# Kernel tuning notes

Hardware: AMD Instinct MI355X
Metric: run time of the kernel (lower is better)

## Reference

```python
import jax, jax.numpy as jnp
import numpy as np
from jax import lax

B, C, H, W = 16, 256, 32, 32
DH = 32
HEADS = C // DH          # 8
WSZ = 4                  # window size
K = 4                    # top-k windows
MR = 4                   # mlp_ratio
NWIN = (H // WSZ) * (W // WSZ)  # 64
WS = WSZ * WSZ                  # 16 tokens per window
EPS = 1e-5


def setup_inputs() -> dict:
    key = jax.random.key(0)
    ks = jax.random.split(key, 8)
    w = lambda i, shape: jax.random.normal(ks[i], shape, jnp.float32) * 0.02
    d = {
        'x': jax.random.normal(ks[0], (B, C, H, W), jnp.float32),
        'bn0_g': jax.random.uniform(ks[1], (C,), jnp.float32, 0.5, 1.5),
        'bn0_b': jnp.zeros((C,), jnp.float32),
        'bn0_m': jnp.zeros((C,), jnp.float32),
        'bn0_v': jnp.ones((C,), jnp.float32),
        'w_qkv': w(2, (3 * C, C)),
        'w_merge': w(3, (C, C)),
        'b_merge': jnp.zeros((C,), jnp.float32),
        'w1': w(4, (MR * C, C)),
        'bn1_g': jax.random.uniform(ks[5], (MR * C,), jnp.float32, 0.5, 1.5),
        'bn1_b': jnp.zeros((MR * C,), jnp.float32),
        'bn1_m': jnp.zeros((MR * C,), jnp.float32),
        'bn1_v': jnp.ones((MR * C,), jnp.float32),
        'dw': w(6, (MR * C, 1, 3, 3)),
        'bn2_g': jax.random.uniform(ks[7], (MR * C,), jnp.float32, 0.5, 1.5),
        'bn2_b': jnp.zeros((MR * C,), jnp.float32),
        'bn2_m': jnp.zeros((MR * C,), jnp.float32),
        'bn2_v': jnp.ones((MR * C,), jnp.float32),
        'w2': w(0, (C, MR * C)),
        'bn3_g': jax.random.uniform(ks[1], (C,), jnp.float32, 0.5, 1.5),
        'bn3_b': jnp.zeros((C,), jnp.float32),
        'bn3_m': jnp.zeros((C,), jnp.float32),
        'bn3_v': jnp.ones((C,), jnp.float32),
    }
    return d


def _bn(x, g, b, m, v):
    # eval-mode BatchNorm2d on NCHW
    s = (g / jnp.sqrt(v + EPS))
    return (x - m[None, :, None, None]) * s[None, :, None, None] + b[None, :, None, None]


def _win(t):
    # [B, C, H, W] -> [B, HEADS, NWIN, WS, DH]
    nh, nw = H // WSZ, W // WSZ
    t = t.reshape(B, HEADS, DH, nh, WSZ, nw, WSZ)
    return t.transpose(0, 1, 3, 5, 4, 6, 2).reshape(B, HEADS, NWIN, WS, DH)


def _unwin(t):
    # [B, HEADS, NWIN, WS, DH] -> [B, C, H, W]
    nh, nw = H // WSZ, W // WSZ
    t = t.reshape(B, HEADS, nh, nw, WSZ, WSZ, DH)
    return t.transpose(0, 1, 6, 2, 4, 3, 5).reshape(B, C, H, W)


def _forward(x, bn0_g, bn0_b, bn0_m, bn0_v, w_qkv, w_merge, b_merge,
             w1, bn1_g, bn1_b, bn1_m, bn1_v, dw, bn2_g, bn2_b, bn2_m, bn2_v,
             w2, bn3_g, bn3_b, bn3_m, bn3_v):
    # qkv projection: BN -> GELU -> 1x1 conv (no bias)
    h = jax.nn.gelu(_bn(x, bn0_g, bn0_b, bn0_m, bn0_v), approximate=False)
    qkv = jnp.einsum('oc,bchw->bohw', w_qkv, h)
    q, k, v = jnp.split(qkv, 3, axis=1)

    qw, kw, vw = _win(q), _win(k), _win(v)  # [B,H,NWIN,WS,DH]
    scale = 1.0 / jnp.sqrt(jnp.float32(DH))

    # window-level descriptors -> window-window affinity -> top-k selection
    wsc = jnp.einsum('bhid,bhjd->bhij', qw.mean(3), kw.mean(3)) * scale
    idx = lax.top_k(wsc, K)[1]  # [B,H,NWIN,K]

    # gather top-k kv windows per query window (irregular access)
    gather = jax.vmap(jax.vmap(lambda t, ix: t[ix]))  # over B, HEADS
    kk = gather(kw, idx).reshape(B, HEADS, NWIN, K * WS, DH)
    vv = gather(vw, idx).reshape(B, HEADS, NWIN, K * WS, DH)

    attn = jax.nn.softmax(jnp.einsum('bhnqd,bhnkd->bhnqk', qw, kk) * scale, axis=-1)
    msg = jnp.einsum('bhnqk,bhnkd->bhnqd', attn, vv)
    msg = _unwin(msg)

    # merge (1x1 conv with bias) + residual
    x = x + jnp.einsum('oc,bchw->bohw', w_merge, msg) + b_merge[None, :, None, None]

    # MB mlp: 1x1 expand -> BN -> GELU -> depthwise 3x3 -> BN -> GELU -> 1x1 -> BN
    h = jnp.einsum('oc,bchw->bohw', w1, x)
    h = jax.nn.gelu(_bn(h, bn1_g, bn1_b, bn1_m, bn1_v), approximate=False)
    h = lax.conv_general_dilated(h, dw, (1, 1), 'SAME',
                                 feature_group_count=MR * C,
                                 dimension_numbers=('NCHW', 'OIHW', 'NCHW'))
    h = jax.nn.gelu(_bn(h, bn2_g, bn2_b, bn2_m, bn2_v), approximate=False)
    h = jnp.einsum('oc,bchw->bohw', w2, h)
    h = _bn(h, bn3_g, bn3_b, bn3_m, bn3_v)
    return x + h


def reference(x, bn0_g, bn0_b, bn0_m, bn0_v, w_qkv, w_merge, b_merge,
              w1, bn1_g, bn1_b, bn1_m, bn1_v, dw, bn2_g, bn2_b, bn2_m, bn2_v,
              w2, bn3_g, bn3_b, bn3_m, bn3_v):
    return _forward(x, bn0_g, bn0_b, bn0_m, bn0_v, w_qkv, w_merge, b_merge,
                    w1, bn1_g, bn1_b, bn1_m, bn1_v, dw, bn2_g, bn2_b, bn2_m, bn2_v,
                    w2, bn3_g, bn3_b, bn3_m, bn3_v)
```

## Files before the change

### kernel.cpp

```cpp
#include <hip/hip_runtime.h>
#include <hip/hip_bf16.h>

#define EPSV 1e-5f

typedef short bf16x8 __attribute__((ext_vector_type(8)));
typedef float f32x4 __attribute__((ext_vector_type(4)));

__device__ __forceinline__ float gelu_f(float x) {
    return 0.5f * x * (1.0f + erff(x * 0.70710678118654752f));
}
__device__ __forceinline__ float b2f(unsigned short u) {
    union { float f; unsigned i; } c; c.i = ((unsigned)u) << 16; return c.f;
}
__device__ __forceinline__ unsigned short f2b(float f) {
    __hip_bfloat16 h = __float2bfloat16(f);
    return *reinterpret_cast<unsigned short*>(&h);
}
__device__ __forceinline__ float lo16f(unsigned v) {
    union { float f; unsigned i; } c; c.i = v << 16; return c.f;
}
__device__ __forceinline__ float hi16f(unsigned v) {
    union { float f; unsigned i; } c; c.i = v & 0xffff0000u; return c.f;
}
__device__ __forceinline__ void gload16(const unsigned short* g, unsigned short* l) {
    __builtin_amdgcn_global_load_lds(
        (const __attribute__((address_space(1))) void*)g,
        (__attribute__((address_space(3))) void*)l, 16, 0, 0);
}

__global__ __launch_bounds__(256) void wcvt_k(const float* __restrict__ w,
                                              unsigned short* __restrict__ o, int n4) {
    int i = blockIdx.x * 256 + threadIdx.x;
    if (i >= n4) return;
    float4 v = ((const float4*)w)[i];
    ushort4 u = make_ushort4(f2b(v.x), f2b(v.y), f2b(v.z), f2b(v.w));
    ((ushort4*)o)[i] = u;
}

__global__ __launch_bounds__(256) void wprep_k(const float* __restrict__ wdw,
    const float* __restrict__ g, const float* __restrict__ bt,
    const float* __restrict__ mu, const float* __restrict__ va,
    float* __restrict__ wt, float* __restrict__ scf, float* __restrict__ shf) {
    int ch = blockIdx.x * 256 + threadIdx.x;
    #pragma unroll
    for (int tap = 0; tap < 9; ++tap)
        wt[tap * 1024 + ch] = wdw[ch * 9 + tap];
    float s = g[ch] * rsqrtf(va[ch] + EPSV);
    scf[ch] = s;
    shf[ch] = bt[ch] - mu[ch] * s;
}

__global__ __launch_bounds__(256) void bn0tr_k(const float* __restrict__ x,
    const float* __restrict__ g, const float* __restrict__ bt,
    const float* __restrict__ mu, const float* __restrict__ va,
    unsigned short* __restrict__ h0b, float* __restrict__ xt) {
    __shared__ float tile[64][65];
    int hw0 = blockIdx.x * 64, c0 = blockIdx.y * 64, b = blockIdx.z;
    int t = threadIdx.x;
    int cl = t >> 6, hl = t & 63;
    #pragma unroll
    for (int r = 0; r < 16; ++r)
        tile[r * 4 + cl][hl] = x[((size_t)(b * 256 + c0 + r * 4 + cl)) * 1024 + hw0 + hl];
    __syncthreads();
    int c = c0 + (t & 63);
    float s = g[c] * rsqrtf(va[c] + EPSV);
    float m_ = mu[c], be = bt[c];
    #pragma unroll
    for (int r = 0; r < 16; ++r) {
        int hl2 = r * 4 + (t >> 6);
        float v = tile[t & 63][hl2];
        size_t o = ((size_t)(b * 1024 + hw0 + hl2)) * 256 + c;
        xt[o] = v;
        h0b[o] = f2b(gelu_f((v - m_) * s + be));
    }
}

__global__ __launch_bounds__(256) void hm_k(const float* __restrict__ xt,
    const float* __restrict__ g, const float* __restrict__ bt,
    const float* __restrict__ mu, const float* __restrict__ va,
    float* __restrict__ hm) {
    int blk = blockIdx.x;
    int b = blk >> 6, win = blk & 63;
    int c = threadIdx.x;
    int base = (win >> 3) * 128 + (win & 7) * 4;
    float s = g[c] * rsqrtf(va[c] + EPSV);
    float m_ = mu[c], be = bt[c];
    float acc = 0.f;
    #pragma unroll
    for (int ty = 0; ty < 4; ++ty)
        #pragma unroll
        for (int tx = 0; tx < 4; ++tx) {
            float v = xt[((size_t)(b * 1024 + base + ty * 32 + tx)) * 256 + c];
            acc += gelu_f((v - m_) * s + be);
        }
    hm[(size_t)blk * 256 + c] = acc * (1.f / 16.f);
}

template <int MODE>
__global__ __launch_bounds__(256) void mgemm(
    const unsigned short* __restrict__ A, const unsigned short* __restrict__ X,
    unsigned short* __restrict__ outb, float* __restrict__ outf,
    const float* __restrict__ res,
    const float* __restrict__ p0, const float* __restrict__ p1,
    const float* __restrict__ p2, const float* __restrict__ p3,
    int M, int Kd) {
    __shared__ __align__(16) unsigned short As[4096];
    __shared__ __align__(16) unsigned short Bs[4096];
    const int t = threadIdx.x;
    const int wid = t >> 6, lane = t & 63;
    const int n0 = blockIdx.x * 128, m0 = blockIdx.y * 128, b = blockIdx.z;
    const unsigned short* Ab = A + (size_t)m0 * Kd;
    const unsigned short* Xb = X + ((size_t)b * 1024 + n0) * Kd;

    const int srow = lane >> 2;
    const int skb  = (lane & 3) * 8;
    const int wr = wid >> 1, wc = wid & 1;
    const int lr = lane & 15;
    const int lk = (lane >> 4) * 8;

    f32x4 acc[4][4] = {};

    for (int k0 = 0; k0 < Kd; k0 += 32) {
        #pragma unroll
        for (int i = 0; i < 2; ++i) {
            int chunk = wid * 2 + i;
            int row = chunk * 16 + srow;
            gload16(Ab + (size_t)row * Kd + k0 + skb, &As[chunk * 512]);
            gload16(Xb + (size_t)row * Kd + k0 + skb, &Bs[chunk * 512]);
        }
        __syncthreads();
        bf16x8 af[4], bfv[4];
        #pragma unroll
        for (int mi = 0; mi < 4; ++mi)
            af[mi] = *(const bf16x8*)&As[(wr * 64 + mi * 16 + lr) * 32 + lk];
        #pragma unroll
        for (int ni = 0; ni < 4; ++ni)
            bfv[ni] = *(const bf16x8*)&Bs[(wc * 64 + ni * 16 + lr) * 32 + lk];
        #pragma unroll
        for (int mi = 0; mi < 4; ++mi)
            #pragma unroll
            for (int ni = 0; ni < 4; ++ni)
                acc[mi][ni] = __builtin_amdgcn_mfma_f32_16x16x32_bf16(
                    af[mi], bfv[ni], acc[mi][ni], 0, 0, 0);
        __syncthreads();
    }

    const int crow = (lane >> 4) * 4;
    #pragma unroll
    for (int ni = 0; ni < 4; ++ni) {
        const int n = n0 + wc * 64 + ni * 16 + lr;
        #pragma unroll
        for (int mi = 0; mi < 4; ++mi) {
            const int m = m0 + wr * 64 + mi * 16 + crow;
            f32x4 v = acc[mi][ni];
            size_t o = ((size_t)b * 1024 + n) * (size_t)M + m;
            if (MODE == 0) {
                *(ushort4*)(outb + o) = make_ushort4(f2b(v[0]), f2b(v[1]), f2b(v[2]), f2b(v[3]));
            } else if (MODE == 1) {
                float4 r = *(const float4*)(res + o);
                float4 bi = *(const float4*)(p0 + m);
                float w0 = v[0] + r.x + bi.x, w1 = v[1] + r.y + bi.y;
                float w2 = v[2] + r.z + bi.z, w3 = v[3] + r.w + bi.w;
                *(float4*)(outf + o) = make_float4(w0, w1, w2, w3);
                *(ushort4*)(outb + o) = make_ushort4(f2b(w0), f2b(w1), f2b(w2), f2b(w3));
            } else if (MODE == 2) {
                float4 gg = *(const float4*)(p0 + m);
                float4 be = *(const float4*)(p1 + m);
                float4 mm = *(const float4*)(p2 + m);
                float4 vv = *(const float4*)(p3 + m);
                float h0 = gelu_f((v[0] - mm.x) * (gg.x * rsqrtf(vv.x + EPSV)) + be.x);
                float h1 = gelu_f((v[1] - mm.y) * (gg.y * rsqrtf(vv.y + EPSV)) + be.y);
                float h2 = gelu_f((v[2] - mm.z) * (gg.z * rsqrtf(vv.z + EPSV)) + be.z);
                float h3 = gelu_f((v[3] - mm.w) * (gg.w * rsqrtf(vv.w + EPSV)) + be.w);
                *(ushort4*)(outb + o) = make_ushort4(f2b(h0), f2b(h1), f2b(h2), f2b(h3));
            } else {
                float4 gg = *(const float4*)(p0 + m);
                float4 be = *(const float4*)(p1 + m);
                float4 mm = *(const float4*)(p2 + m);
                float4 vv = *(const float4*)(p3 + m);
                float4 r = *(const float4*)(res + o);
                float y0 = (v[0] - mm.x) * (gg.x * rsqrtf(vv.x + EPSV)) + be.x + r.x;
                float y1 = (v[1] - mm.y) * (gg.y * rsqrtf(vv.y + EPSV)) + be.y + r.y;
                float y2 = (v[2] - mm.z) * (gg.z * rsqrtf(vv.z + EPSV)) + be.z + r.z;
                float y3 = (v[3] - mm.w) * (gg.w * rsqrtf(vv.w + EPSV)) + be.w + r.w;
                *(float4*)(outf + o) = make_float4(y0, y1, y2, y3);
            }
        }
    }
}

__global__ __launch_bounds__(256) void topk2_k(const float* __restrict__ hm,
                                               const float* __restrict__ w_qkv,
                                               int* __restrict__ idx_out) {
    int bh = blockIdx.x; int b = bh >> 3, h = bh & 7;
    __shared__ float hmc[64][33];
    __shared__ float wqc[32][33];
    __shared__ float wkc[32][33];
    __shared__ float qm[64][33];
    __shared__ float km[64][33];
    __shared__ float wsc[64][65];
    int t = threadIdx.x;
    const float* hb = hm + (size_t)b * 64 * 256;
    const float* wq = w_qkv + (size_t)(h * 32) * 256;
    const float* wk = w_qkv + (size_t)(256 + h * 32) * 256;
    int win = t >> 2;
    int db  = (t & 3) * 8;
    float aq[8] = {0,0,0,0,0,0,0,0}, ak[8] = {0,0,0,0,0,0,0,0};
    for (int c0 = 0; c0 < 256; c0 += 32) {
        for (int e = t; e < 2048; e += 256) {
            int wn = e >> 5, cc = e & 31;
            hmc[wn][cc] = hb[wn * 256 + c0 + cc];
        }
        for (int e = t; e < 1024; e += 256) {
            int d = e >> 5, cc = e & 31;
            wqc[d][cc] = wq[d * 256 + c0 + cc];
            wkc[d][cc] = wk[d * 256 + c0 + cc];
        }
        __syncthreads();
        #pragma unroll
        for (int cc = 0; cc < 32; ++cc) {
            float hv = hmc[win][cc];
            #pragma unroll
            for (int j = 0; j < 8; ++j) {
                aq[j] += wqc[db + j][cc] * hv;
                ak[j] += wkc[db + j][cc] * hv;
            }
        }
        __syncthreads();
    }
    #pragma unroll
    for (int j = 0; j < 8; ++j) { qm[win][db + j] = aq[j]; km[win][db + j] = ak[j]; }
    __syncthreads();
    for (int e = t; e < 4096; e += 256) {
        int i = e >> 6, j = e & 63;
        float s = 0.f;
        #pragma unroll
        for (int d = 0; d < 32; ++d) s += qm[i][d] * km[j][d];
        wsc[i][j] = s;
    }
    __syncthreads();
    if (t < 64) {
        float bv[4] = {-1e30f, -1e30f, -1e30f, -1e30f};
        int   bi[4] = {0, 0, 0, 0};
        for (int j = 0; j < 64; ++j) {
            float v = wsc[t][j];
            if (v > bv[3]) {
                int p = 3;
                while (p > 0 && v > bv[p - 1]) {
                    bv[p] = bv[p - 1]; bi[p] = bi[p - 1]; --p;
                }
                bv[p] = v; bi[p] = j;
            }
        }
        int* o = idx_out + (bh * 64 + t) * 4;
        o[0] = bi[0]; o[1] = bi[1]; o[2] = bi[2]; o[3] = bi[3];
    }
}

__global__ __launch_bounds__(256) void attn_k(const unsigned short* __restrict__ qkv,
                                              const int* __restrict__ idx,
                                              unsigned short* __restrict__ msg) {
    int blk = blockIdx.x;
    int win = blk & 63;
    int bh = blk >> 6;
    int b = bh >> 3, h = bh & 7;
    __shared__ float qs[16][32];
    __shared__ float ks[64][32];
    __shared__ float vs[64][32];
    __shared__ float sc[16][64];
    __shared__ int widx[4];
    int t = threadIdx.x;
    if (t < 4) widx[t] = idx[(bh * 64 + win) * 4 + t];
    __syncthreads();
    int qb = (win >> 3) * 128 + (win & 7) * 4;
    for (int e = t; e < 512; e += 256) {
        int tok = e >> 5, d = e & 31;
        int hw = qb + (tok >> 2) * 32 + (tok & 3);
        qs[tok][d] = b2f(qkv[((size_t)(b * 1024 + hw)) * 768 + h * 32 + d]);
    }
    for (int e = t; e < 2048; e += 256) {
        int key = e >> 5, d = e & 31;
        int wsel = widx[key >> 4];
        int tok = key & 15;
        int hw = (wsel >> 3) * 128 + (wsel & 7) * 4 + (tok >> 2) * 32 + (tok & 3);
        size_t base = ((size_t)(b * 1024 + hw)) * 768 + h * 32 + d;
        ks[key][d] = b2f(qkv[base + 256]);
        vs[key][d] = b2f(qkv[base + 512]);
    }
    __syncthreads();
    const float scale = 0.17677669529663688f;
    for (int e = t; e < 1024; e += 256) {
        int r = e >> 6, cidx = e & 63;
        float s = 0.f;
        #pragma unroll
        for (int d = 0; d < 32; ++d) s += qs[r][d] * ks[cidx][d];
        sc[r][cidx] = s * scale;
    }
    __syncthreads();
    {
        int r = t >> 4, c0 = (t & 15) << 2;
        float v0 = sc[r][c0], v1 = sc[r][c0 + 1], v2 = sc[r][c0 + 2], v3 = sc[r][c0 + 3];
        float mx = fmaxf(fmaxf(v0, v1), fmaxf(v2, v3));
        #pragma unroll
        for (int m = 1; m < 16; m <<= 1) mx = fmaxf(mx, __shfl_xor(mx, m));
        float e0 = expf(v0 - mx), e1 = expf(v1 - mx), e2 = expf(v2 - mx), e3 = expf(v3 - mx);
        float sm = e0 + e1 + e2 + e3;
        #pragma unroll
        for (int m = 1; m < 16; m <<= 1) sm += __shfl_xor(sm, m);
        float inv = 1.0f / sm;
        sc[r][c0] = e0 * inv; sc[r][c0 + 1] = e1 * inv;
        sc[r][c0 + 2] = e2 * inv; sc[r][c0 + 3] = e3 * inv;
    }
    __syncthreads();
    for (int e = t; e < 512; e += 256) {
        int tok = e >> 5, d = e & 31;
        float s = 0.f;
        #pragma unroll
        for (int kk = 0; kk < 64; ++kk) s += sc[tok][kk] * vs[kk][d];
        int hw = qb + (tok >> 2) * 32 + (tok & 3);
        msg[((size_t)(b * 1024 + hw)) * 256 + h * 32 + d] = f2b(s);
    }
}

__global__ __launch_bounds__(256) void dw_k(const unsigned short* __restrict__ h1,
    const float* __restrict__ wt, const float* __restrict__ scf,
    const float* __restrict__ shf, unsigned short* __restrict__ h2) {
    int t = threadIdx.x;
    int c8 = t & 127;
    int pl = t >> 7;
    int blk = blockIdx.x;
    int b = blk >> 7;
    int rem = blk & 127;
    int y = rem >> 2;
    int x0 = (rem & 3) * 8;
    int ch0 = c8 * 8;

    float w[9][8];
    #pragma unroll
    for (int tap = 0; tap < 9; ++tap) {
        float4 a = *(const float4*)(wt + tap * 1024 + ch0);
        float4 bq = *(const float4*)(wt + tap * 1024 + ch0 + 4);
        w[tap][0] = a.x; w[tap][1] = a.y; w[tap][2] = a.z; w[tap][3] = a.w;
        w[tap][4] = bq.x; w[tap][5] = bq.y; w[tap][6] = bq.z; w[tap][7] = bq.w;
    }
    float sc[8], sh[8];
    {
        float4 a = *(const float4*)(scf + ch0);
        float4 bq = *(const float4*)(scf + ch0 + 4);
        sc[0]=a.x; sc[1]=a.y; sc[2]=a.z; sc[3]=a.w; sc[4]=bq.x; sc[5]=bq.y; sc[6]=bq.z; sc[7]=bq.w;
        float4 c = *(const float4*)(shf + ch0);
        float4 dq = *(const float4*)(shf + ch0 + 4);
        sh[0]=c.x; sh[1]=c.y; sh[2]=c.z; sh[3]=c.w; sh[4]=dq.x; sh[5]=dq.y; sh[6]=dq.z; sh[7]=dq.w;
    }

    const unsigned short* base = h1 + (size_t)b * 1048576;
    unsigned short* ob = h2 + (size_t)b * 1048576;

    #pragma unroll
    for (int j = 0; j < 4; ++j) {
        int x = x0 + pl + 2 * j;
        float acc[8] = {0.f,0.f,0.f,0.f,0.f,0.f,0.f,0.f};
        #pragma unroll
        for (int dy = -1; dy <= 1; ++dy) {
            int yy = y + dy;
            if (yy < 0 || yy > 31) continue;
            #pragma unroll
            for (int dx = -1; dx <= 1; ++dx) {
                int xx = x + dx;
                if (xx < 0 || xx > 31) continue;
                uint4 u = *(const uint4*)(base + (size_t)(yy * 32 + xx) * 1024 + ch0);
                int tap = (dy + 1) * 3 + (dx + 1);
                acc[0] += lo16f(u.x) * w[tap][0];
                acc[1] += hi16f(u.x) * w[tap][1];
                acc[2] += lo16f(u.y) * w[tap][2];
                acc[3] += hi16f(u.y) * w[tap][3];
                acc[4] += lo16f(u.z) * w[tap][4];
                acc[5] += hi16f(u.z) * w[tap][5];
                acc[6] += lo16f(u.w) * w[tap][6];
                acc[7] += hi16f(u.w) * w[tap][7];
            }
        }
        unsigned short r[8];
        #pragma unroll
        for (int c = 0; c < 8; ++c)
            r[c] = f2b(gelu_f(acc[c] * sc[c] + sh[c]));
        uint4 o;
        o.x = (unsigned)r[0] | ((unsigned)r[1] << 16);
        o.y = (unsigned)r[2] | ((unsigned)r[3] << 16);
        o.z = (unsigned)r[4] | ((unsigned)r[5] << 16);
        o.w = (unsigned)r[6] | ((unsigned)r[7] << 16);
        *(uint4*)(ob + (size_t)(y * 32 + x) * 1024 + ch0) = o;
    }
}

__global__ __launch_bounds__(256) void trout_k(const float* __restrict__ y,
                                               float* __restrict__ out) {
    __shared__ float tile[64][65];
    int hw0 = blockIdx.x * 64, c0 = blockIdx.y * 64, b = blockIdx.z;
    int t = threadIdx.x;
    #pragma unroll
    for (int r = 0; r < 16; ++r) {
        int hl = r * 4 + (t >> 6);
        tile[t & 63][hl] = y[((size_t)(b * 1024 + hw0 + hl)) * 256 + c0 + (t & 63)];
    }
    __syncthreads();
    #pragma unroll
    for (int r = 0; r < 16; ++r) {
        int cl = r * 4 + (t >> 6);
        out[((size_t)(b * 256 + c0 + cl)) * 1024 + hw0 + (t & 63)] = tile[cl][t & 63];
    }
}

extern "C" void kernel_launch(void* const* d_in, const int* in_sizes, int n_in,
                              void* d_out, int out_size, void* d_ws, size_t ws_size,
                              hipStream_t stream) {
    const float* x      = (const float*)d_in[0];
    const float* bn0_g  = (const float*)d_in[1];
    const float* bn0_b  = (const float*)d_in[2];
    const float* bn0_m  = (const float*)d_in[3];
    const float* bn0_v  = (const float*)d_in[4];
    const float* w_qkv  = (const float*)d_in[5];
    const float* w_merge= (const float*)d_in[6];
    const float* b_merge= (const float*)d_in[7];
    const float* w1     = (const float*)d_in[8];
    const float* bn1_g  = (const float*)d_in[9];
    const float* bn1_b  = (const float*)d_in[10];
    const float* bn1_m  = (const float*)d_in[11];
    const float* bn1_v  = (const float*)d_in[12];
    const float* dw     = (const float*)d_in[13];
    const float* bn2_g  = (const float*)d_in[14];
    const float* bn2_b  = (const float*)d_in[15];
    const float* bn2_m  = (const float*)d_in[16];
    const float* bn2_v  = (const float*)d_in[17];
    const float* w2     = (const float*)d_in[18];
    const float* bn3_g  = (const float*)d_in[19];
    const float* bn3_b  = (const float*)d_in[20];
    const float* bn3_m  = (const float*)d_in[21];
    const float* bn3_v  = (const float*)d_in[22];
    float* out = (float*)d_out;

    char* w = (char*)d_ws;
    unsigned short* h0b   = (unsigned short*)(w);
    unsigned short* qkvb  = (unsigned short*)(w + 8388608);
    unsigned short* msgb  = (unsigned short*)(w + 33554432);
    unsigned short* xrb   = (unsigned short*)(w + 41943040);
    unsigned short* h1b   = (unsigned short*)(w + 50331648);
    unsigned short* h2b   = (unsigned short*)(w + 83886080);
    float*  xt    = (float*)(w + 117440512);
    float*  xrf   = (float*)(w + 134217728);
    float*  yf    = (float*)(w + 150994944);
    float*  hm    = (float*)(w + 167772160);
    unsigned short* wqkvb = (unsigned short*)(w + 168820736);
    unsigned short* wmrgb = (unsigned short*)(w + 169213952);
    unsigned short* w1b   = (unsigned short*)(w + 169345024);
    unsigned short* w2b   = (unsigned short*)(w + 169869312);
    int*    idx   = (int*)(w + 170393600);
    float*  wtbuf = (float*)(w + 170524672);
    float*  scbuf = (float*)(w + 170561536);
    float*  shbuf = (float*)(w + 170565632);

    wcvt_k<<<192, 256, 0, stream>>>(w_qkv, wqkvb, 49152);
    wcvt_k<<<64,  256, 0, stream>>>(w_merge, wmrgb, 16384);
    wcvt_k<<<256, 256, 0, stream>>>(w1, w1b, 65536);
    wcvt_k<<<256, 256, 0, stream>>>(w2, w2b, 65536);
    wprep_k<<<4, 256, 0, stream>>>(dw, bn2_g, bn2_b, bn2_m, bn2_v, wtbuf, scbuf, shbuf);

    bn0tr_k<<<dim3(16, 4, 16), 256, 0, stream>>>(x, bn0_g, bn0_b, bn0_m, bn0_v, h0b, xt);
    hm_k<<<1024, 256, 0, stream>>>(xt, bn0_g, bn0_b, bn0_m, bn0_v, hm);
    mgemm<0><<<dim3(8, 6, 16), 256, 0, stream>>>(wqkvb, h0b, qkvb, nullptr,
        nullptr, nullptr, nullptr, nullptr, nullptr, 768, 256);
    topk2_k<<<128, 256, 0, stream>>>(hm, w_qkv, idx);
    attn_k<<<8192, 256, 0, stream>>>(qkvb, idx, msgb);
    mgemm<1><<<dim3(8, 2, 16), 256, 0, stream>>>(wmrgb, msgb, xrb, xrf,
        xt, b_merge, nullptr, nullptr, nullptr, 256, 256);
    mgemm<2><<<dim3(8, 8, 16), 256, 0, stream>>>(w1b, xrb, h1b, nullptr,
        nullptr, bn1_g, bn1_b, bn1_m, bn1_v, 1024, 256);
    dw_k<<<2048, 256, 0, stream>>>(h1b, wtbuf, scbuf, shbuf, h2b);
    mgemm<3><<<dim3(8, 2, 16), 256, 0, stream>>>(w2b, h2b, nullptr, yf,
        xrf, bn3_g, bn3_b, bn3_m, bn3_v, 256, 1024);
    trout_k<<<dim3(16, 4, 16), 256, 0, stream>>>(yf, out);
}
```

Baseline: 405.0 us.

## Split top-k routing kernel into parallel descriptor and affinity kernels

The single 128-block top-k kernel, which projected window means to q/k descriptors and computed window affinities, is split into two kernels. A new 1024-block kernel computes the q and k descriptors, one thread per output channel. A slimmer 128-block kernel loads those descriptors and computes affinities with register tiling before the top-4 selection. The aim is to expose more parallelism for the projection, at the cost of an extra launch and a global round-trip for the descriptors.

Result: slower. 449.0 us (+10.9%).

```diff
diff --git a/kernel.cpp b/kernel.cpp
--- a/kernel.cpp
+++ b/kernel.cpp
@@ -189,54 +189,60 @@
     }
 }
 
-__global__ __launch_bounds__(256) void topk2_k(const float* __restrict__ hm,
-                                               const float* __restrict__ w_qkv,
-                                               int* __restrict__ idx_out) {
-    int bh = blockIdx.x; int b = bh >> 3, h = bh & 7;
-    __shared__ float hmc[64][33];
-    __shared__ float wqc[32][33];
-    __shared__ float wkc[32][33];
-    __shared__ float qm[64][33];
-    __shared__ float km[64][33];
+__global__ __launch_bounds__(256) void desc_k(const float* __restrict__ hm,
+                                              const float* __restrict__ w_qkv,
+                                              float* __restrict__ qd,
+                                              float* __restrict__ kd) {
+    int blk = blockIdx.x;
+    __shared__ float hrow[256];
+    int t = threadIdx.x;
+    hrow[t] = hm[(size_t)blk * 256 + t];
+    __syncthreads();
+    const float4* wq = (const float4*)(w_qkv + (size_t)t * 256);
+    const float4* wk = (const float4*)(w_qkv + (size_t)(256 + t) * 256);
+    float sq = 0.f, sk = 0.f;
+    #pragma unroll 8
+    for (int c4 = 0; c4 < 64; ++c4) {
+        float4 a = wq[c4];
+        float4 b = wk[c4];
+        float h0 = hrow[c4 * 4], h1 = hrow[c4 * 4 + 1];
+        float h2 = hrow[c4 * 4 + 2], h3 = hrow[c4 * 4 + 3];
+        sq += a.x * h0 + a.y * h1 + a.z * h2 + a.w * h3;
+        sk += b.x * h0 + b.y * h1 + b.z * h2 + b.w * h3;
+    }
+    qd[(size_t)blk * 256 + t] = sq;
+    kd[(size_t)blk * 256 + t] = sk;
+}
+
+__global__ __launch_bounds__(256) void aff_k(const float* __restrict__ qd,
+                                             const float* __restrict__ kd,
+                                             int* __restrict__ idx_out) {
+    int bh = blockIdx.x;
+    int b = bh >> 3, h = bh & 7;
+    __shared__ float qdl[64][33];
+    __shared__ float kdl[64][33];
     __shared__ float wsc[64][65];
     int t = threadIdx.x;
-    const float* hb = hm + (size_t)b * 64 * 256;
-    const float* wq = w_qkv + (size_t)(h * 32) * 256;
-    const float* wk = w_qkv + (size_t)(256 + h * 32) * 256;
-    int win = t >> 2;
-    int db  = (t & 3) * 8;
-    float aq[8] = {0,0,0,0,0,0,0,0}, ak[8] = {0,0,0,0,0,0,0,0};
-    for (int c0 = 0; c0 < 256; c0 += 32) {
-        for (int e = t; e < 2048; e += 256) {
-            int wn = e >> 5, cc = e & 31;
-            hmc[wn][cc] = hb[wn * 256 + c0 + cc];
-        }
-        for (int e = t; e < 1024; e += 256) {
-            int d = e >> 5, cc = e & 31;
-            wqc[d][cc] = wq[d * 256 + c0 + cc];
-            wkc[d][cc] = wk[d * 256 + c0 + cc];
-        }
-        __syncthreads();
-        #pragma unroll
-        for (int cc = 0; cc < 32; ++cc) {
-            float hv = hmc[win][cc];
+    for (int e = t; e < 2048; e += 256) {
+        int wn = e >> 5, d = e & 31;
+        size_t src = ((size_t)(b * 64 + wn)) * 256 + h * 32 + d;
+        qdl[wn][d] = qd[src];
+        kdl[wn][d] = kd[src];
+    }
+    __syncthreads();
+    {
+        int i = t >> 2, j0 = (t & 3) * 16;
+        float s[16];
+        #pragma unroll
+        for (int j = 0; j < 16; ++j) s[j] = 0.f;
+        #pragma unroll
+        for (int d = 0; d < 32; ++d) {
+            float qv = qdl[i][d];
             #pragma unroll
-            for (int j = 0; j < 8; ++j) {
-                aq[j] += wqc[db + j][cc] * hv;
-                ak[j] += wkc[db + j][cc] * hv;
-            }
-        }
-        __syncthreads();
-    }
-    #pragma unroll
-    for (int j = 0; j < 8; ++j) { qm[win][db + j] = aq[j]; km[win][db + j] = ak[j]; }
-    __syncthreads();
-    for (int e = t; e < 4096; e += 256) {
-        int i = e >> 6, j = e & 63;
-        float s = 0.f;
-        #pragma unroll
-        for (int d = 0; d < 32; ++d) s += qm[i][d] * km[j][d];
-        wsc[i][j] = s;
+            for (int j = 0; j < 16; ++j) s[j] += qv * kdl[j0 + j][d];
+        }
+        #pragma unroll
+        for (int j = 0; j < 16; ++j) wsc[i][j0 + j] = s[j];
     }
     __syncthreads();
     if (t < 64) {
@@ -458,6 +464,8 @@
     float*  wtbuf = (float*)(w + 170524672);
     float*  scbuf = (float*)(w + 170561536);
     float*  shbuf = (float*)(w + 170565632);
+    float*  qdbuf = (float*)(w + 170569728);
+    float*  kdbuf = (float*)(w + 171618304);
 
     wcvt_k<<<192, 256, 0, stream>>>(w_qkv, wqkvb, 49152);
     wcvt_k<<<64,  256, 0, stream>>>(w_merge, wmrgb, 16384);
@@ -469,7 +477,8 @@
     hm_k<<<1024, 256, 0, stream>>>(xt, bn0_g, bn0_b, bn0_m, bn0_v, hm);
     mgemm<0><<<dim3(8, 6, 16), 256, 0, stream>>>(wqkvb, h0b, qkvb, nullptr,
         nullptr, nullptr, nullptr, nullptr, nullptr, 768, 256);
-    topk2_k<<<128, 256, 0, stream>>>(hm, w_qkv, idx);
+    desc_k<<<1024, 256, 0, stream>>>(hm, w_qkv, qdbuf, kdbuf);
+    aff_k<<<128, 256, 0, stream>>>(qdbuf, kdbuf, idx);
     attn_k<<<8192, 256, 0, stream>>>(qkvb, idx, msgb);
     mgemm<1><<<dim3(8, 2, 16), 256, 0, stream>>>(wmrgb, msgb, xrb, xrf,
         xt, b_merge, nullptr, nullptr, nullptr, 256, 256);
```
